# Kernel tuning notes

Hardware: AMD Instinct MI355X
Metric: run time of the kernel (lower is better)

## Reference

```python
import jax, jax.numpy as jnp
import numpy as np

N_GRAPHS = 128
N_NODES = 512
N = N_GRAPHS * N_NODES      # 65536 total nodes
E = 524288                  # edges (avg degree 8)
F_IN = 4                    # num_features
EMB = 4                     # embedding_dim
HEADS = 4
GDIM = 16                   # GATConv_dim
D = GDIM * HEADS            # 64 = d_model
NHEAD = 2                   # heads // 2
FF = 64                     # ff_hid_dim
OUT = 64                    # output_dim
N_GAT_REST = 3              # gat_layers - 1


def setup_inputs() -> dict:
    key = jax.random.key(0)
    ks = iter(jax.random.split(key, 64))
    def nrm(shape, fan_in):
        return jax.random.normal(next(ks), shape, jnp.float32) / np.float32(np.sqrt(fan_in))
    inp = {}
    inp['x'] = jax.random.normal(next(ks), (N, F_IN), jnp.float32)
    inp['edge_index'] = jax.random.randint(next(ks), (2, E), 0, N, dtype=jnp.int32)
    inp['batch'] = jnp.repeat(jnp.arange(N_GRAPHS, dtype=jnp.int32), N_NODES)
    # feature_fc
    inp['Wf'] = nrm((F_IN, EMB), F_IN); inp['bf'] = jnp.zeros((EMB,), jnp.float32)
    # input GATConv (EMB -> HEADS*GDIM)
    inp['gW0'] = nrm((EMB, HEADS * GDIM), EMB)
    inp['aS0'] = nrm((HEADS, GDIM), GDIM); inp['aD0'] = nrm((HEADS, GDIM), GDIM)
    inp['gb0'] = jnp.zeros((D,), jnp.float32)
    # remaining 3 GATConv layers (D -> HEADS*GDIM), stacked
    inp['gW'] = nrm((N_GAT_REST, D, HEADS * GDIM), D)
    inp['aS'] = nrm((N_GAT_REST, HEADS, GDIM), GDIM); inp['aD'] = nrm((N_GAT_REST, HEADS, GDIM), GDIM)
    inp['gb'] = jnp.zeros((N_GAT_REST, D), jnp.float32)
    # decoder layer: self-attn, cross-attn, layernorms, FFN
    for p in ['sWq','sWk','sWv','sWo','cWq','cWk','cWv','cWo']:
        inp[p] = nrm((D, D), D)
    for p in ['sbq','sbk','sbv','sbo','cbq','cbk','cbv','cbo']:
        inp[p] = jnp.zeros((D,), jnp.float32)
    for g, b in [('ln1g','ln1b'), ('ln2g','ln2b'), ('ln3g','ln3b')]:
        inp[g] = jnp.ones((D,), jnp.float32); inp[b] = jnp.zeros((D,), jnp.float32)
    inp['ffW1'] = nrm((D, FF), D); inp['ffb1'] = jnp.zeros((FF,), jnp.float32)
    inp['ffW2'] = nrm((FF, D), FF); inp['ffb2'] = jnp.zeros((D,), jnp.float32)
    inp['fcW'] = nrm((D, OUT), D); inp['fcb'] = jnp.zeros((OUT,), jnp.float32)
    return inp


def _gat(h_in, src, dst, W, a_s, a_d, b):
    # PyG GATConv, concat=True, negative_slope=0.2, self-loops already in (src,dst)
    h = (h_in @ W).reshape(N, HEADS, GDIM)
    es = jnp.einsum('nho,ho->nh', h, a_s)   # [N,H]
    ed = jnp.einsum('nho,ho->nh', h, a_d)
    e = jax.nn.leaky_relu(es[src] + ed[dst], 0.2)          # [E',H]
    m = jax.ops.segment_max(e, dst, num_segments=N)        # segment softmax over dst
    w = jnp.exp(e - m[dst])
    s = jax.ops.segment_sum(w, dst, num_segments=N)
    alpha = w / (s[dst] + 1e-16)
    out = jax.ops.segment_sum(h[src] * alpha[..., None], dst, num_segments=N)
    return out.reshape(N, D) + b


def _mha(q, kv, Wq, bq, Wk, bk, Wv, bv, Wo, bo):
    B, S, Dm = q.shape
    hd = Dm // NHEAD
    Q = (q @ Wq + bq).reshape(B, S, NHEAD, hd)
    K = (kv @ Wk + bk).reshape(B, S, NHEAD, hd)
    V = (kv @ Wv + bv).reshape(B, S, NHEAD, hd)
    a = jax.nn.softmax(jnp.einsum('bqhd,bkhd->bhqk', Q, K) / jnp.sqrt(jnp.float32(hd)), axis=-1)
    o = jnp.einsum('bhqk,bkhd->bqhd', a, V).reshape(B, S, Dm)
    return o @ Wo + bo


def _ln(x, g, b):
    m = x.mean(-1, keepdims=True)
    v = ((x - m) ** 2).mean(-1, keepdims=True)
    return (x - m) / jnp.sqrt(v + 1e-5) * g + b


def reference(x, edge_index, batch, Wf, bf, gW0, aS0, aD0, gb0, gW, aS, aD, gb,
              sWq, sWk, sWv, sWo, cWq, cWk, cWv, cWo,
              sbq, sbk, sbv, sbo, cbq, cbk, cbv, cbo,
              ln1g, ln1b, ln2g, ln2b, ln3g, ln3b,
              ffW1, ffb1, ffW2, ffb2, fcW, fcb):
    loops = jnp.arange(N, dtype=edge_index.dtype)
    src = jnp.concatenate([edge_index[0], loops])
    dst = jnp.concatenate([edge_index[1], loops])
    h = x @ Wf + bf
    h = jax.nn.leaky_relu(_gat(h, src, dst, gW0, aS0, aD0, gb0), 0.01)
    for i in range(N_GAT_REST):
        h = jax.nn.leaky_relu(_gat(h, src, dst, gW[i], aS[i], aD[i], gb[i]), 0.01)
    t = h.reshape(N_GRAPHS, N_NODES, D)
    # one transformer decoder layer, post-norm, memory = layer input
    mem = t
    t = _ln(t + _mha(t, t, sWq, sbq, sWk, sbk, sWv, sbv, sWo, sbo), ln1g, ln1b)
    t = _ln(t + _mha(t, mem, cWq, cbq, cWk, cbk, cWv, cbv, cWo, cbo), ln2g, ln2b)
    t = _ln(t + (jax.nn.relu(t @ ffW1 + ffb1) @ ffW2 + ffb2), ln3g, ln3b)
    h = t.reshape(N, D)
    pooled = jax.ops.segment_sum(h, batch, num_segments=N_GRAPHS) / jnp.float32(N_NODES)
    return pooled @ fcW + fcb
```

## Files before the change

### kernel.cpp

```cpp
#include <hip/hip_runtime.h>
#include <math.h>

#define NG 128
#define SEQ 512
#define NN 65536
#define EE 524288
#define DM 64

typedef __attribute__((ext_vector_type(8))) short short8;
typedef __attribute__((ext_vector_type(4))) float f32x4;

__device__ __forceinline__ float lrelu(float x, float s){ return x > 0.f ? x : s*x; }

__device__ __forceinline__ unsigned short f2bf(float x){
  union { float f; unsigned u; } v; v.f = x;
  unsigned r = v.u + 0x7FFF + ((v.u>>16)&1);
  return (unsigned short)(r>>16);
}
__device__ __forceinline__ float bf2f(unsigned short x){
  union { unsigned u; float f; } v; v.u = ((unsigned)x)<<16;
  return v.f;
}

__global__ void k_count(const int* __restrict__ dst, int* __restrict__ deg){
  int e = blockIdx.x*256 + threadIdx.x;
  atomicAdd(&deg[dst[e]], 1);
}

__global__ void k_scan1(const int* __restrict__ deg, int* __restrict__ excl, int* __restrict__ bsums){
  __shared__ int sm[256];
  int tid = threadIdx.x;
  int i = blockIdx.x*256 + tid;
  int v = deg[i];
  sm[tid] = v;
  __syncthreads();
  int val = v;
  for (int off=1; off<256; off<<=1){
    int add = (tid>=off)? sm[tid-off] : 0;
    __syncthreads();
    val += add;
    sm[tid] = val;
    __syncthreads();
  }
  excl[i] = val - v;
  if (tid==255) bsums[blockIdx.x] = val;
}

__global__ void k_scan2(int* __restrict__ bsums){
  __shared__ int sm[256];
  int tid=threadIdx.x;
  int v = bsums[tid];
  sm[tid]=v;
  __syncthreads();
  int val=v;
  for (int off=1; off<256; off<<=1){
    int add = (tid>=off)? sm[tid-off]:0;
    __syncthreads();
    val += add;
    sm[tid]=val;
    __syncthreads();
  }
  bsums[tid] = val - v;
}

__global__ void k_scan3(const int* __restrict__ excl, const int* __restrict__ bsums,
                        int* __restrict__ rowp, int* __restrict__ cursor){
  int i = blockIdx.x*256 + threadIdx.x;
  int v = excl[i] + bsums[blockIdx.x];
  rowp[i]=v; cursor[i]=v;
  if (i==0) rowp[NN]=EE;
}

__global__ void k_fill(const int* __restrict__ src, const int* __restrict__ dst,
                       int* __restrict__ cursor, int* __restrict__ col){
  int e = blockIdx.x*256 + threadIdx.x;
  int d = dst[e];
  int p = atomicAdd(&cursor[d], 1);
  col[p] = src[e];
}

__global__ void k_w0(const float* __restrict__ Wf, const float* __restrict__ bf,
                     const float* __restrict__ gW0, float* __restrict__ W0c, float* __restrict__ b0c){
  int j = threadIdx.x;
  float b = 0.f;
  for (int k=0;k<4;k++) b += bf[k]*gW0[k*64+j];
  b0c[j]=b;
  for (int i=0;i<4;i++){
    float s=0.f;
    for(int k=0;k<4;k++) s += Wf[i*4+k]*gW0[k*64+j];
    W0c[i*64+j]=s;
  }
}

template<int DIN, int BIAS>
__global__ void __launch_bounds__(256) k_transform(const float* __restrict__ hin, const float* __restrict__ W,
                            const float* __restrict__ bias,
                            const float* __restrict__ aSp, const float* __restrict__ aDp,
                            unsigned short* __restrict__ hout, float* __restrict__ es, float* __restrict__ ed){
  __shared__ float inL[DIN][68];
  __shared__ float Wl[DIN][64];
  __shared__ float asl[64], adl[64];
  int tid = threadIdx.x;
  int n0 = blockIdx.x*64;
  if (tid < 64){ asl[tid] = aSp[tid]; adl[tid] = aDp[tid]; }
  for (int idx=tid; idx<DIN*16; idx+=256){
    int k = idx>>4, jj = (idx&15)<<2;
    *(float4*)&Wl[k][jj] = *(const float4*)&W[k*64+jj];
  }
  for (int idx=tid; idx<64*(DIN/4); idx+=256){
    int node = idx/(DIN/4), kk = (idx%(DIN/4))*4;
    float4 v = *(const float4*)&hin[(size_t)(n0+node)*DIN + kk];
    inL[kk][node]=v.x; inL[kk+1][node]=v.y; inL[kk+2][node]=v.z; inL[kk+3][node]=v.w;
  }
  __syncthreads();
  int i = tid>>4, j = tid&15;
  float acc[4][4];
  #pragma unroll
  for (int r=0;r<4;r++){
    #pragma unroll
    for (int c=0;c<4;c++) acc[r][c] = 0.f;
  }
  #pragma unroll 4
  for (int k=0;k<DIN;k++){
    float4 av = *(float4*)&inL[k][4*i];
    float4 bv = *(float4*)&Wl[k][4*j];
    float a_[4]={av.x,av.y,av.z,av.w}, b_[4]={bv.x,bv.y,bv.z,bv.w};
    #pragma unroll
    for (int r=0;r<4;r++){
      #pragma unroll
      for (int c=0;c<4;c++) acc[r][c] += a_[r]*b_[c];
    }
  }
  float4 asv = *(float4*)&asl[4*j];
  float4 adv = *(float4*)&adl[4*j];
  float bb[4] = {0.f,0.f,0.f,0.f};
  if (BIAS){
    float4 bv = *(const float4*)&bias[4*j];
    bb[0]=bv.x; bb[1]=bv.y; bb[2]=bv.z; bb[3]=bv.w;
  }
  #pragma unroll
  for (int r=0;r<4;r++){
    float y0=acc[r][0]+bb[0], y1=acc[r][1]+bb[1], y2=acc[r][2]+bb[2], y3=acc[r][3]+bb[3];
    int node = n0 + 4*i + r;
    ushort4 hv;
    hv.x=f2bf(y0); hv.y=f2bf(y1); hv.z=f2bf(y2); hv.w=f2bf(y3);
    *(ushort4*)&hout[(size_t)node*64 + 4*j] = hv;
    float ps = y0*asv.x + y1*asv.y + y2*asv.z + y3*asv.w;
    float pd = y0*adv.x + y1*adv.y + y2*adv.z + y3*adv.w;
    ps += __shfl_xor(ps,1); ps += __shfl_xor(ps,2);
    pd += __shfl_xor(pd,1); pd += __shfl_xor(pd,2);
    if ((j&3)==0){
      es[(size_t)node*4 + (j>>2)] = ps;
      ed[(size_t)node*4 + (j>>2)] = pd;
    }
  }
}

__global__ void __launch_bounds__(256) k_aggregate(const unsigned short* __restrict__ h, const float* __restrict__ es,
                            const float* __restrict__ ed, const int* __restrict__ rowp,
                            const int* __restrict__ col, const float* __restrict__ gb,
                            float* __restrict__ hout){
  int tid = threadIdx.x;
  int n = blockIdx.x*4 + (tid>>6);
  int lane = tid&63;
  int hh = lane>>4;
  float edn = ed[(size_t)n*4 + hh];
  int beg = rowp[n], end = rowp[n+1];
  float m = lrelu(es[(size_t)n*4+hh] + edn, 0.2f);
  float ssum = 1.f;
  float acc = bf2f(h[(size_t)n*64 + lane]);
  int i = beg;
  for (; i+4 <= end; i += 4){
    int s0 = col[i], s1 = col[i+1], s2 = col[i+2], s3 = col[i+3];
    float hv0 = bf2f(h[(size_t)s0*64 + lane]);
    float hv1 = bf2f(h[(size_t)s1*64 + lane]);
    float hv2 = bf2f(h[(size_t)s2*64 + lane]);
    float hv3 = bf2f(h[(size_t)s3*64 + lane]);
    float e0 = lrelu(es[(size_t)s0*4+hh] + edn, 0.2f);
    float e1 = lrelu(es[(size_t)s1*4+hh] + edn, 0.2f);
    float e2 = lrelu(es[(size_t)s2*4+hh] + edn, 0.2f);
    float e3 = lrelu(es[(size_t)s3*4+hh] + edn, 0.2f);
    float mx = fmaxf(fmaxf(e0,e1), fmaxf(e2,e3));
    if (mx > m + 8.f){
      float corr = __expf(m - mx);
      ssum *= corr; acc *= corr; m = mx;
    }
    float w0 = __expf(e0 - m), w1 = __expf(e1 - m);
    float w2 = __expf(e2 - m), w3 = __expf(e3 - m);
    ssum += (w0 + w1) + (w2 + w3);
    acc += (w0*hv0 + w1*hv1) + (w2*hv2 + w3*hv3);
  }
  for (; i < end; i++){
    int s0 = col[i];
    float hv0 = bf2f(h[(size_t)s0*64 + lane]);
    float e0 = lrelu(es[(size_t)s0*4+hh] + edn, 0.2f);
    if (e0 > m + 8.f){
      float corr = __expf(m - e0);
      ssum *= corr; acc *= corr; m = e0;
    }
    float w0 = __expf(e0 - m);
    ssum += w0;
    acc += w0*hv0;
  }
  float o = acc/(ssum + 1e-16f) + gb[lane];
  hout[(size_t)n*64 + lane] = lrelu(o, 0.01f);
}

template<int ACT>
__global__ void __launch_bounds__(256) k_linear(const float* __restrict__ in, const float* __restrict__ W,
                         const float* __restrict__ b, float* __restrict__ out){
  __shared__ float inL[64][68];
  __shared__ float Wl[64][64];
  int tid = threadIdx.x;
  int n0 = blockIdx.x*64;
  for (int idx=tid; idx<1024; idx+=256){
    int k = idx>>4, jj = (idx&15)<<2;
    *(float4*)&Wl[k][jj] = *(const float4*)&W[k*64+jj];
  }
  for (int idx=tid; idx<1024; idx+=256){
    int node = idx>>4, kk = (idx&15)<<2;
    float4 v = *(const float4*)&in[(size_t)(n0+node)*64 + kk];
    inL[kk][node]=v.x; inL[kk+1][node]=v.y; inL[kk+2][node]=v.z; inL[kk+3][node]=v.w;
  }
  __syncthreads();
  int i = tid>>4, j = tid&15;
  float acc[4][4];
  #pragma unroll
  for (int r=0;r<4;r++){
    #pragma unroll
    for (int c=0;c<4;c++) acc[r][c] = 0.f;
  }
  #pragma unroll 4
  for (int k=0;k<64;k++){
    float4 av = *(float4*)&inL[k][4*i];
    float4 bv = *(float4*)&Wl[k][4*j];
    float a_[4]={av.x,av.y,av.z,av.w}, b_[4]={bv.x,bv.y,bv.z,bv.w};
    #pragma unroll
    for (int r=0;r<4;r++){
      #pragma unroll
      for (int c=0;c<4;c++) acc[r][c] += a_[r]*b_[c];
    }
  }
  float4 bv = *(const float4*)&b[4*j];
  float bb[4] = {bv.x, bv.y, bv.z, bv.w};
  #pragma unroll
  for (int r=0;r<4;r++){
    float y[4];
    #pragma unroll
    for (int c=0;c<4;c++){
      y[c] = acc[r][c] + bb[c];
      if (ACT==1) y[c] = fmaxf(y[c], 0.f);
    }
    *(float4*)&out[(size_t)(n0+4*i+r)*64 + 4*j] = make_float4(y[0],y[1],y[2],y[3]);
  }
}

__global__ void __launch_bounds__(256) k_qkv(const float* __restrict__ in,
                      const float* __restrict__ W0, const float* __restrict__ b0, float* __restrict__ o0,
                      const float* __restrict__ W1, const float* __restrict__ b1, float* __restrict__ o1,
                      const float* __restrict__ W2, const float* __restrict__ b2, float* __restrict__ o2){
  __shared__ float inL[64][68];
  __shared__ float Wl[64][64];
  int tid = threadIdx.x;
  int n0 = blockIdx.x*64;
  for (int idx=tid; idx<1024; idx+=256){
    int node = idx>>4, kk = (idx&15)<<2;
    float4 v = *(const float4*)&in[(size_t)(n0+node)*64 + kk];
    inL[kk][node]=v.x; inL[kk+1][node]=v.y; inL[kk+2][node]=v.z; inL[kk+3][node]=v.w;
  }
  int i = tid>>4, j = tid&15;
  const float* Ws[3] = {W0, W1, W2};
  const float* bs[3] = {b0, b1, b2};
  float* os[3] = {o0, o1, o2};
  for (int w=0; w<3; w++){
    __syncthreads();
    for (int idx=tid; idx<1024; idx+=256){
      int k = idx>>4, jj = (idx&15)<<2;
      *(float4*)&Wl[k][jj] = *(const float4*)&Ws[w][k*64+jj];
    }
    __syncthreads();
    float acc[4][4];
    #pragma unroll
    for (int r=0;r<4;r++){
      #pragma unroll
      for (int c=0;c<4;c++) acc[r][c] = 0.f;
    }
    #pragma unroll 4
    for (int k=0;k<64;k++){
      float4 av = *(float4*)&inL[k][4*i];
      float4 bv = *(float4*)&Wl[k][4*j];
      float a_[4]={av.x,av.y,av.z,av.w}, b_[4]={bv.x,bv.y,bv.z,bv.w};
      #pragma unroll
      for (int r=0;r<4;r++){
        #pragma unroll
        for (int c=0;c<4;c++) acc[r][c] += a_[r]*b_[c];
      }
    }
    float4 bv = *(const float4*)&bs[w][4*j];
    float bb[4] = {bv.x, bv.y, bv.z, bv.w};
    #pragma unroll
    for (int r=0;r<4;r++){
      *(float4*)&os[w][(size_t)(n0+4*i+r)*64 + 4*j] =
        make_float4(acc[r][0]+bb[0], acc[r][1]+bb[1], acc[r][2]+bb[2], acc[r][3]+bb[3]);
    }
  }
}

__global__ void __launch_bounds__(256) k_kv(const float* __restrict__ in,
                     const float* __restrict__ W0, const float* __restrict__ b0, float* __restrict__ o0,
                     const float* __restrict__ W1, const float* __restrict__ b1, float* __restrict__ o1){
  __shared__ float inL[64][68];
  __shared__ float Wl[64][64];
  int tid = threadIdx.x;
  int n0 = blockIdx.x*64;
  for (int idx=tid; idx<1024; idx+=256){
    int node = idx>>4, kk = (idx&15)<<2;
    float4 v = *(const float4*)&in[(size_t)(n0+node)*64 + kk];
    inL[kk][node]=v.x; inL[kk+1][node]=v.y; inL[kk+2][node]=v.z; inL[kk+3][node]=v.w;
  }
  int i = tid>>4, j = tid&15;
  const float* Ws[2] = {W0, W1};
  const float* bs[2] = {b0, b1};
  float* os[2] = {o0, o1};
  for (int w=0; w<2; w++){
    __syncthreads();
    for (int idx=tid; idx<1024; idx+=256){
      int k = idx>>4, jj = (idx&15)<<2;
      *(float4*)&Wl[k][jj] = *(const float4*)&Ws[w][k*64+jj];
    }
    __syncthreads();
    float acc[4][4];
    #pragma unroll
    for (int r=0;r<4;r++){
      #pragma unroll
      for (int c=0;c<4;c++) acc[r][c] = 0.f;
    }
    #pragma unroll 4
    for (int k=0;k<64;k++){
      float4 av = *(float4*)&inL[k][4*i];
      float4 bv = *(float4*)&Wl[k][4*j];
      float a_[4]={av.x,av.y,av.z,av.w}, b_[4]={bv.x,bv.y,bv.z,bv.w};
      #pragma unroll
      for (int r=0;r<4;r++){
        #pragma unroll
        for (int c=0;c<4;c++) acc[r][c] += a_[r]*b_[c];
      }
    }
    float4 bv = *(const float4*)&bs[w][4*j];
    float bb[4] = {bv.x, bv.y, bv.z, bv.w};
    #pragma unroll
    for (int r=0;r<4;r++){
      *(float4*)&os[w][(size_t)(n0+4*i+r)*64 + 4*j] =
        make_float4(acc[r][0]+bb[0], acc[r][1]+bb[1], acc[r][2]+bb[2], acc[r][3]+bb[3]);
    }
  }
}

__global__ void __launch_bounds__(256) k_linear_resln(const float* __restrict__ in, const float* __restrict__ W,
                               const float* __restrict__ b, const float* __restrict__ res,
                               const float* __restrict__ g, const float* __restrict__ bl,
                               float* __restrict__ out){
  __shared__ float inL[64][68];
  __shared__ float Wl[64][64];
  int tid = threadIdx.x;
  int n0 = blockIdx.x*64;
  for (int idx=tid; idx<1024; idx+=256){
    int k = idx>>4, jj = (idx&15)<<2;
    *(float4*)&Wl[k][jj] = *(const float4*)&W[k*64+jj];
  }
  for (int idx=tid; idx<1024; idx+=256){
    int node = idx>>4, kk = (idx&15)<<2;
    float4 v = *(const float4*)&in[(size_t)(n0+node)*64 + kk];
    inL[kk][node]=v.x; inL[kk+1][node]=v.y; inL[kk+2][node]=v.z; inL[kk+3][node]=v.w;
  }
  __syncthreads();
  int i = tid>>4, j = tid&15;
  float acc[4][4];
  #pragma unroll
  for (int r=0;r<4;r++){
    #pragma unroll
    for (int c=0;c<4;c++) acc[r][c] = 0.f;
  }
  #pragma unroll 4
  for (int k=0;k<64;k++){
    float4 av = *(float4*)&inL[k][4*i];
    float4 bv = *(float4*)&Wl[k][4*j];
    float a_[4]={av.x,av.y,av.z,av.w}, b_[4]={bv.x,bv.y,bv.z,bv.w};
    #pragma unroll
    for (int r=0;r<4;r++){
      #pragma unroll
      for (int c=0;c<4;c++) acc[r][c] += a_[r]*b_[c];
    }
  }
  float4 bv = *(const float4*)&b[4*j];
  float bb[4] = {bv.x, bv.y, bv.z, bv.w};
  float4 gv = *(const float4*)&g[4*j];
  float4 blv = *(const float4*)&bl[4*j];
  float gg[4] = {gv.x, gv.y, gv.z, gv.w};
  float bb2[4] = {blv.x, blv.y, blv.z, blv.w};
  #pragma unroll
  for (int r=0;r<4;r++){
    int node = n0 + 4*i + r;
    float4 rv = *(const float4*)&res[(size_t)node*64 + 4*j];
    float y[4] = {acc[r][0]+bb[0]+rv.x, acc[r][1]+bb[1]+rv.y,
                  acc[r][2]+bb[2]+rv.z, acc[r][3]+bb[3]+rv.w};
    float s = (y[0]+y[1]) + (y[2]+y[3]);
    s += __shfl_xor(s,1); s += __shfl_xor(s,2); s += __shfl_xor(s,4); s += __shfl_xor(s,8);
    float mean = s * (1.f/64.f);
    float d[4] = {y[0]-mean, y[1]-mean, y[2]-mean, y[3]-mean};
    float v = (d[0]*d[0]+d[1]*d[1]) + (d[2]*d[2]+d[3]*d[3]);
    v += __shfl_xor(v,1); v += __shfl_xor(v,2); v += __shfl_xor(v,4); v += __shfl_xor(v,8);
    float inv = rsqrtf(v*(1.f/64.f) + 1e-5f);
    *(float4*)&out[(size_t)node*64 + 4*j] =
      make_float4(d[0]*inv*gg[0]+bb2[0], d[1]*inv*gg[1]+bb2[1],
                  d[2]*inv*gg[2]+bb2[2], d[3]*inv*gg[3]+bb2[3]);
  }
}

__global__ void __launch_bounds__(512, 4) k_attn(const float* __restrict__ Q, const float* __restrict__ K,
                      const float* __restrict__ V, float* __restrict__ Out){
  __shared__ char smem[40960];
  char* Ksm = smem;
  char* Vsm = smem + 16384;
  char* Psm = smem + 32768;

  int bid = blockIdx.x;
  int qh = bid & 1;
  int h  = (bid>>1) & 1;
  int b  = bid>>2;
  int tid = threadIdx.x;
  int wave = tid>>6;
  int l = tid & 63;
  int lq = l & 15;
  int g  = l >> 4;
  const float scale = 0.17677669529663687f;
  const size_t hb = (size_t)b*SEQ*64 + (size_t)h*32;
  const f32x4 zero = {0.f,0.f,0.f,0.f};

  int qbase = qh*256 + wave*32;
  short8 qf[2];
  f32x4 O[2][2];
  float m_[2], l_[2];
  #pragma unroll
  for (int qt=0; qt<2; qt++){
    const float* qp = Q + hb + (size_t)(qbase + qt*16 + lq)*64 + g*8;
    float4 a = *(const float4*)qp;
    float4 c = *(const float4*)(qp+4);
    union { short8 v; unsigned short u[8]; } uu;
    uu.u[0]=f2bf(a.x*scale); uu.u[1]=f2bf(a.y*scale); uu.u[2]=f2bf(a.z*scale); uu.u[3]=f2bf(a.w*scale);
    uu.u[4]=f2bf(c.x*scale); uu.u[5]=f2bf(c.y*scale); uu.u[6]=f2bf(c.z*scale); uu.u[7]=f2bf(c.w*scale);
    qf[qt] = uu.v;
    O[qt][0] = zero; O[qt][1] = zero;
    m_[qt] = -1e30f; l_[qt] = 0.f;
  }

  char* Pw = Psm + wave*1024;

  for (int ph=0; ph<2; ph++){
    __syncthreads();
    #pragma unroll
    for (int it=0; it<4; it++){
      int i = tid + it*512;
      int row = i>>3, j = i&7;
      const float* kp = K + hb + (size_t)(ph*256 + row)*64 + j*4;
      float4 v4 = *(const float4*)kp;
      uint2 w;
      w.x = (unsigned)f2bf(v4.x) | ((unsigned)f2bf(v4.y)<<16);
      w.y = (unsigned)f2bf(v4.z) | ((unsigned)f2bf(v4.w)<<16);
      *(uint2*)(Ksm + row*64 + ((j*8) ^ (((row>>1)&3)<<4))) = w;
    }
    #pragma unroll
    for (int it=0; it<4; it++){
      int i = tid + it*512;
      int key = i>>3, j = i&7;
      const float* vp = V + hb + (size_t)(ph*256 + key)*64 + j*4;
      float4 v4 = *(const float4*)vp;
      float vv[4] = {v4.x, v4.y, v4.z, v4.w};
      #pragma unroll
      for (int c=0;c<4;c++){
        int d = j*4 + c;
        *(unsigned short*)(Vsm + d*512 + ((key*2) ^ ((d&7)<<4))) = f2bf(vv[c]);
      }
    }
    __syncthreads();
    for (int p=0; p<8; p++){
      int r0 = p*32 + lq, r1 = r0 + 16;
      short8 kf0 = *(short8*)(Ksm + r0*64 + ((g*16) ^ (((r0>>1)&3)<<4)));
      short8 kf1 = *(short8*)(Ksm + r1*64 + ((g*16) ^ (((r1>>1)&3)<<4)));
      int d0 = lq, d1 = lq + 16;
      short8 vt0 = *(short8*)(Vsm + d0*512 + ((p*64 + g*16) ^ ((d0&7)<<4)));
      short8 vt1 = *(short8*)(Vsm + d1*512 + ((p*64 + g*16) ^ ((d1&7)<<4)));
      int swzp = ((lq>>1)&3)<<4;
      #pragma unroll
      for (int qt=0; qt<2; qt++){
        f32x4 s0 = __builtin_amdgcn_mfma_f32_16x16x32_bf16(kf0, qf[qt], zero, 0,0,0);
        f32x4 s1 = __builtin_amdgcn_mfma_f32_16x16x32_bf16(kf1, qf[qt], zero, 0,0,0);
        float pmax = fmaxf(fmaxf(fmaxf(s0.x,s0.y),fmaxf(s0.z,s0.w)),
                           fmaxf(fmaxf(s1.x,s1.y),fmaxf(s1.z,s1.w)));
        pmax = fmaxf(pmax, __shfl_xor(pmax, 16));
        pmax = fmaxf(pmax, __shfl_xor(pmax, 32));
        float mn = fmaxf(m_[qt], pmax);
        float corr = __expf(m_[qt] - mn);
        m_[qt] = mn;
        float e0 = __expf(s0.x - mn), e1 = __expf(s0.y - mn);
        float e2 = __expf(s0.z - mn), e3 = __expf(s0.w - mn);
        float e4 = __expf(s1.x - mn), e5 = __expf(s1.y - mn);
        float e6 = __expf(s1.z - mn), e7 = __expf(s1.w - mn);
        l_[qt] = l_[qt]*corr + (((e0+e1)+(e2+e3)) + ((e4+e5)+(e6+e7)));
        O[qt][0] *= corr; O[qt][1] *= corr;
        uint2 w0, w1;
        w0.x = (unsigned)f2bf(e0) | ((unsigned)f2bf(e1)<<16);
        w0.y = (unsigned)f2bf(e2) | ((unsigned)f2bf(e3)<<16);
        w1.x = (unsigned)f2bf(e4) | ((unsigned)f2bf(e5)<<16);
        w1.y = (unsigned)f2bf(e6) | ((unsigned)f2bf(e7)<<16);
        *(uint2*)(Pw + lq*64 + ((g*8) ^ swzp)) = w0;
        *(uint2*)(Pw + lq*64 + ((32 + g*8) ^ swzp)) = w1;
        short8 pb = *(short8*)(Pw + lq*64 + ((g*16) ^ swzp));
        O[qt][0] = __builtin_amdgcn_mfma_f32_16x16x32_bf16(vt0, pb, O[qt][0], 0,0,0);
        O[qt][1] = __builtin_amdgcn_mfma_f32_16x16x32_bf16(vt1, pb, O[qt][1], 0,0,0);
      }
    }
  }
  #pragma unroll
  for (int qt=0; qt<2; qt++){
    float lt = l_[qt];
    lt += __shfl_xor(lt, 16);
    lt += __shfl_xor(lt, 32);
    float inv = 1.f/lt;
    float* op = Out + hb + (size_t)(qbase + qt*16 + lq)*64;
    float4 o0 = make_float4(O[qt][0].x*inv, O[qt][0].y*inv, O[qt][0].z*inv, O[qt][0].w*inv);
    float4 o1 = make_float4(O[qt][1].x*inv, O[qt][1].y*inv, O[qt][1].z*inv, O[qt][1].w*inv);
    *(float4*)(op + g*4) = o0;
    *(float4*)(op + 16 + g*4) = o1;
  }
}

__global__ void __launch_bounds__(256) k_pool_fc(const float* __restrict__ t, const float* __restrict__ fcW,
                          const float* __restrict__ fcb, float* __restrict__ out){
  __shared__ float pl[4][64];
  __shared__ float pf[64];
  int b = blockIdx.x;
  int tid = threadIdx.x;
  int j = tid&63, seg = tid>>6;
  const float* basep = t + (size_t)b*SEQ*64;
  float s = 0.f;
  for (int si=seg*128; si<(seg+1)*128; si++) s += basep[(size_t)si*64 + j];
  pl[seg][j] = s;
  __syncthreads();
  if (tid < 64){
    pf[tid] = (pl[0][tid]+pl[1][tid]+pl[2][tid]+pl[3][tid]) * (1.f/512.f);
  }
  __syncthreads();
  if (tid < 64){
    float o = fcb[tid];
    for (int k=0;k<64;k++) o += pf[k]*fcW[k*64+tid];
    out[(size_t)b*64 + tid] = o;
  }
}

extern "C" void kernel_launch(void* const* d_in, const int* in_sizes, int n_in,
                              void* d_out, int out_size, void* d_ws, size_t ws_size,
                              hipStream_t stream) {
  const float* x    = (const float*)d_in[0];
  const int*   ei   = (const int*)d_in[1];
  const float* Wf   = (const float*)d_in[3];
  const float* bf   = (const float*)d_in[4];
  const float* gW0  = (const float*)d_in[5];
  const float* aS0  = (const float*)d_in[6];
  const float* aD0  = (const float*)d_in[7];
  const float* gb0  = (const float*)d_in[8];
  const float* gW   = (const float*)d_in[9];
  const float* aS   = (const float*)d_in[10];
  const float* aD   = (const float*)d_in[11];
  const float* gb   = (const float*)d_in[12];
  const float* sWq  = (const float*)d_in[13];
  const float* sWk  = (const float*)d_in[14];
  const float* sWv  = (const float*)d_in[15];
  const float* sWo  = (const float*)d_in[16];
  const float* cWq  = (const float*)d_in[17];
  const float* cWk  = (const float*)d_in[18];
  const float* cWv  = (const float*)d_in[19];
  const float* cWo  = (const float*)d_in[20];
  const float* sbq  = (const float*)d_in[21];
  const float* sbk  = (const float*)d_in[22];
  const float* sbv  = (const float*)d_in[23];
  const float* sbo  = (const float*)d_in[24];
  const float* cbq  = (const float*)d_in[25];
  const float* cbk  = (const float*)d_in[26];
  const float* cbv  = (const float*)d_in[27];
  const float* cbo  = (const float*)d_in[28];
  const float* ln1g = (const float*)d_in[29];
  const float* ln1b = (const float*)d_in[30];
  const float* ln2g = (const float*)d_in[31];
  const float* ln2b = (const float*)d_in[32];
  const float* ln3g = (const float*)d_in[33];
  const float* ln3b = (const float*)d_in[34];
  const float* ffW1 = (const float*)d_in[35];
  const float* ffb1 = (const float*)d_in[36];
  const float* ffW2 = (const float*)d_in[37];
  const float* ffb2 = (const float*)d_in[38];
  const float* fcW  = (const float*)d_in[39];
  const float* fcb  = (const float*)d_in[40];

  char* ws = (char*)d_ws;
  size_t off = 0;
  auto alloc = [&](size_t bytes) -> void* {
    void* p = ws + off;
    off += (bytes + 255) & ~(size_t)255;
    return p;
  };
  int* deg    = (int*)alloc(NN*sizeof(int));
  int* excl   = (int*)alloc(NN*sizeof(int));
  int* rowp   = (int*)alloc((NN+1)*sizeof(int));
  int* cursor = (int*)alloc(NN*sizeof(int));
  int* col    = (int*)alloc(EE*sizeof(int));
  int* bsums  = (int*)alloc(256*sizeof(int));
  float* W0c  = (float*)alloc(4*64*sizeof(float));
  float* b0c  = (float*)alloc(64*sizeof(float));
  float* es   = (float*)alloc((size_t)NN*4*sizeof(float));
  float* ed   = (float*)alloc((size_t)NN*4*sizeof(float));
  unsigned short* Hb = (unsigned short*)alloc((size_t)NN*64*sizeof(unsigned short));
  float* B0   = (float*)alloc((size_t)NN*64*sizeof(float));
  float* B1   = (float*)alloc((size_t)NN*64*sizeof(float));
  float* B2   = (float*)alloc((size_t)NN*64*sizeof(float));
  float* B3   = (float*)alloc((size_t)NN*64*sizeof(float));
  float* B4   = (float*)alloc((size_t)NN*64*sizeof(float));
  float* B5   = (float*)alloc((size_t)NN*64*sizeof(float));

  const int* e_src = ei;
  const int* e_dst = ei + EE;

  hipMemsetAsync(deg, 0, NN*sizeof(int), stream);
  k_count<<<EE/256, 256, 0, stream>>>(e_dst, deg);
  k_scan1<<<NN/256, 256, 0, stream>>>(deg, excl, bsums);
  k_scan2<<<1, 256, 0, stream>>>(bsums);
  k_scan3<<<NN/256, 256, 0, stream>>>(excl, bsums, rowp, cursor);
  k_fill<<<EE/256, 256, 0, stream>>>(e_src, e_dst, cursor, col);

  k_w0<<<1, 64, 0, stream>>>(Wf, bf, gW0, W0c, b0c);

  k_transform<4,1><<<NN/64, 256, 0, stream>>>(x, W0c, b0c, aS0, aD0, Hb, es, ed);
  k_aggregate<<<NN/4, 256, 0, stream>>>(Hb, es, ed, rowp, col, gb0, B0);
  k_transform<64,0><<<NN/64, 256, 0, stream>>>(B0, gW+0*4096, nullptr, aS+0*64, aD+0*64, Hb, es, ed);
  k_aggregate<<<NN/4, 256, 0, stream>>>(Hb, es, ed, rowp, col, gb+0*64, B2);
  k_transform<64,0><<<NN/64, 256, 0, stream>>>(B2, gW+1*4096, nullptr, aS+1*64, aD+1*64, Hb, es, ed);
  k_aggregate<<<NN/4, 256, 0, stream>>>(Hb, es, ed, rowp, col, gb+1*64, B0);
  k_transform<64,0><<<NN/64, 256, 0, stream>>>(B0, gW+2*4096, nullptr, aS+2*64, aD+2*64, Hb, es, ed);
  k_aggregate<<<NN/4, 256, 0, stream>>>(Hb, es, ed, rowp, col, gb+2*64, B2);

  k_qkv<<<NN/64, 256, 0, stream>>>(B2, sWq, sbq, B0, sWk, sbk, B1, sWv, sbv, B3);
  k_attn<<<NG*2*2, 512, 0, stream>>>(B0, B1, B3, B4);
  k_linear_resln<<<NN/64, 256, 0, stream>>>(B4, sWo, sbo, B2, ln1g, ln1b, B5);

  k_linear<0><<<NN/64, 256, 0, stream>>>(B5, cWq, cbq, B0);
  k_kv<<<NN/64, 256, 0, stream>>>(B2, cWk, cbk, B1, cWv, cbv, B3);
  k_attn<<<NG*2*2, 512, 0, stream>>>(B0, B1, B3, B4);
  k_linear_resln<<<NN/64, 256, 0, stream>>>(B4, cWo, cbo, B5, ln2g, ln2b, B2);

  k_linear<1><<<NN/64, 256, 0, stream>>>(B2, ffW1, ffb1, B0);
  k_linear_resln<<<NN/64, 256, 0, stream>>>(B0, ffW2, ffb2, B2, ln3g, ln3b, B1);

  k_pool_fc<<<NG, 256, 0, stream>>>(B1, fcW, fcb, (float*)d_out);
}
```

Baseline: 453.8 us.

## Vectorize GAT aggregation across edges, keep intermediates bf16, merge cross-attn projections

The aggregation kernel now assigns four edge slots per wavefront, with 16 lanes each gathering four bf16 features as a ushort4. Partial online-softmax states are merged with shuffles, and the self-loop is folded in at the end. The three intermediate GAT layer outputs are written as bf16 and read by a new bf16-input transform kernel, which halves those memory round trips. The cross-attention Q projection and KV projection are merged into one generalized three-input projection kernel, removing a launch. The aim is fewer dependent gather latencies and less traffic, at the cost of extra bf16 rounding and idle lanes on low-degree nodes.

```diff
diff --git a/kernel.cpp b/kernel.cpp
--- a/kernel.cpp
+++ b/kernel.cpp
@@ -156,54 +156,147 @@
   }
 }
 
+__global__ void __launch_bounds__(256) k_transform_bf(const unsigned short* __restrict__ hin, const float* __restrict__ W,
+                            const float* __restrict__ aSp, const float* __restrict__ aDp,
+                            unsigned short* __restrict__ hout, float* __restrict__ es, float* __restrict__ ed){
+  __shared__ float inL[64][68];
+  __shared__ float Wl[64][64];
+  __shared__ float asl[64], adl[64];
+  int tid = threadIdx.x;
+  int n0 = blockIdx.x*64;
+  if (tid < 64){ asl[tid] = aSp[tid]; adl[tid] = aDp[tid]; }
+  for (int idx=tid; idx<1024; idx+=256){
+    int k = idx>>4, jj = (idx&15)<<2;
+    *(float4*)&Wl[k][jj] = *(const float4*)&W[k*64+jj];
+  }
+  for (int idx=tid; idx<1024; idx+=256){
+    int node = idx>>4, kk = (idx&15)<<2;
+    ushort4 v = *(const ushort4*)&hin[(size_t)(n0+node)*64 + kk];
+    inL[kk][node]=bf2f(v.x); inL[kk+1][node]=bf2f(v.y); inL[kk+2][node]=bf2f(v.z); inL[kk+3][node]=bf2f(v.w);
+  }
+  __syncthreads();
+  int i = tid>>4, j = tid&15;
+  float acc[4][4];
+  #pragma unroll
+  for (int r=0;r<4;r++){
+    #pragma unroll
+    for (int c=0;c<4;c++) acc[r][c] = 0.f;
+  }
+  #pragma unroll 4
+  for (int k=0;k<64;k++){
+    float4 av = *(float4*)&inL[k][4*i];
+    float4 bv = *(float4*)&Wl[k][4*j];
+    float a_[4]={av.x,av.y,av.z,av.w}, b_[4]={bv.x,bv.y,bv.z,bv.w};
+    #pragma unroll
+    for (int r=0;r<4;r++){
+      #pragma unroll
+      for (int c=0;c<4;c++) acc[r][c] += a_[r]*b_[c];
+    }
+  }
+  float4 asv = *(float4*)&asl[4*j];
+  float4 adv = *(float4*)&adl[4*j];
+  #pragma unroll
+  for (int r=0;r<4;r++){
+    float y0=acc[r][0], y1=acc[r][1], y2=acc[r][2], y3=acc[r][3];
+    int node = n0 + 4*i + r;
+    ushort4 hv;
+    hv.x=f2bf(y0); hv.y=f2bf(y1); hv.z=f2bf(y2); hv.w=f2bf(y3);
+    *(ushort4*)&hout[(size_t)node*64 + 4*j] = hv;
+    float ps = y0*asv.x + y1*asv.y + y2*asv.z + y3*asv.w;
+    float pd = y0*adv.x + y1*adv.y + y2*adv.z + y3*adv.w;
+    ps += __shfl_xor(ps,1); ps += __shfl_xor(ps,2);
+    pd += __shfl_xor(pd,1); pd += __shfl_xor(pd,2);
+    if ((j&3)==0){
+      es[(size_t)node*4 + (j>>2)] = ps;
+      ed[(size_t)node*4 + (j>>2)] = pd;
+    }
+  }
+}
+
+template<int BF16OUT>
 __global__ void __launch_bounds__(256) k_aggregate(const unsigned short* __restrict__ h, const float* __restrict__ es,
                             const float* __restrict__ ed, const int* __restrict__ rowp,
                             const int* __restrict__ col, const float* __restrict__ gb,
-                            float* __restrict__ hout){
+                            void* __restrict__ houtv){
   int tid = threadIdx.x;
   int n = blockIdx.x*4 + (tid>>6);
-  int lane = tid&63;
-  int hh = lane>>4;
-  float edn = ed[(size_t)n*4 + hh];
+  int l = tid&63;
+  int q = l>>4;
+  int sl = l&15;
+  int head = sl>>2;
+  float edn = ed[(size_t)n*4 + head];
+  float es_self = es[(size_t)n*4 + head];
   int beg = rowp[n], end = rowp[n+1];
-  float m = lrelu(es[(size_t)n*4+hh] + edn, 0.2f);
-  float ssum = 1.f;
-  float acc = bf2f(h[(size_t)n*64 + lane]);
-  int i = beg;
-  for (; i+4 <= end; i += 4){
-    int s0 = col[i], s1 = col[i+1], s2 = col[i+2], s3 = col[i+3];
-    float hv0 = bf2f(h[(size_t)s0*64 + lane]);
-    float hv1 = bf2f(h[(size_t)s1*64 + lane]);
-    float hv2 = bf2f(h[(size_t)s2*64 + lane]);
-    float hv3 = bf2f(h[(size_t)s3*64 + lane]);
-    float e0 = lrelu(es[(size_t)s0*4+hh] + edn, 0.2f);
-    float e1 = lrelu(es[(size_t)s1*4+hh] + edn, 0.2f);
-    float e2 = lrelu(es[(size_t)s2*4+hh] + edn, 0.2f);
-    float e3 = lrelu(es[(size_t)s3*4+hh] + edn, 0.2f);
-    float mx = fmaxf(fmaxf(e0,e1), fmaxf(e2,e3));
-    if (mx > m + 8.f){
-      float corr = __expf(m - mx);
-      ssum *= corr; acc *= corr; m = mx;
-    }
-    float w0 = __expf(e0 - m), w1 = __expf(e1 - m);
-    float w2 = __expf(e2 - m), w3 = __expf(e3 - m);
-    ssum += (w0 + w1) + (w2 + w3);
-    acc += (w0*hv0 + w1*hv1) + (w2*hv2 + w3*hv3);
-  }
-  for (; i < end; i++){
-    int s0 = col[i];
-    float hv0 = bf2f(h[(size_t)s0*64 + lane]);
-    float e0 = lrelu(es[(size_t)s0*4+hh] + edn, 0.2f);
-    if (e0 > m + 8.f){
-      float corr = __expf(m - e0);
-      ssum *= corr; acc *= corr; m = e0;
-    }
-    float w0 = __expf(e0 - m);
-    ssum += w0;
-    acc += w0*hv0;
-  }
-  float o = acc/(ssum + 1e-16f) + gb[lane];
-  hout[(size_t)n*64 + lane] = lrelu(o, 0.01f);
+  float m = -1e30f, s = 0.f;
+  float a0=0.f, a1=0.f, a2=0.f, a3=0.f;
+  for (int i=beg; i<end; i+=8){
+    int ei0 = i + q, ei1 = i + 4 + q;
+    bool ac0 = ei0 < end, ac1 = ei1 < end;
+    int i0 = ac0 ? ei0 : end-1;
+    int i1 = ac1 ? ei1 : end-1;
+    int s0 = col[i0], s1 = col[i1];
+    ushort4 hv0 = *(const ushort4*)&h[(size_t)s0*64 + 4*sl];
+    ushort4 hv1 = *(const ushort4*)&h[(size_t)s1*64 + 4*sl];
+    float e0 = lrelu(es[(size_t)s0*4+head] + edn, 0.2f);
+    float e1 = lrelu(es[(size_t)s1*4+head] + edn, 0.2f);
+    if (!ac0) e0 = -1e30f;
+    if (!ac1) e1 = -1e30f;
+    float mx = fmaxf(e0, e1);
+    if (__any(mx > m + 8.f)){
+      float nm = fmaxf(m, mx);
+      float c = __expf(m - nm);
+      s*=c; a0*=c; a1*=c; a2*=c; a3*=c; m = nm;
+    }
+    float w0 = ac0 ? __expf(e0 - m) : 0.f;
+    float w1 = ac1 ? __expf(e1 - m) : 0.f;
+    s += w0 + w1;
+    a0 += w0*bf2f(hv0.x) + w1*bf2f(hv1.x);
+    a1 += w0*bf2f(hv0.y) + w1*bf2f(hv1.y);
+    a2 += w0*bf2f(hv0.z) + w1*bf2f(hv1.z);
+    a3 += w0*bf2f(hv0.w) + w1*bf2f(hv1.w);
+  }
+  #pragma unroll
+  for (int off=16; off<=32; off<<=1){
+    float m2 = __shfl_xor(m, off);
+    float s2 = __shfl_xor(s, off);
+    float b0 = __shfl_xor(a0, off);
+    float b1 = __shfl_xor(a1, off);
+    float b2 = __shfl_xor(a2, off);
+    float b3 = __shfl_xor(a3, off);
+    float nm = fmaxf(m, m2);
+    float c1 = __expf(m - nm), c2 = __expf(m2 - nm);
+    s  = s*c1  + s2*c2;
+    a0 = a0*c1 + b0*c2;
+    a1 = a1*c1 + b1*c2;
+    a2 = a2*c1 + b2*c2;
+    a3 = a3*c1 + b3*c2;
+    m = nm;
+  }
+  {
+    float e_self = lrelu(es_self + edn, 0.2f);
+    float nm = fmaxf(m, e_self);
+    float c = __expf(m - nm), cs = __expf(e_self - nm);
+    ushort4 hs = *(const ushort4*)&h[(size_t)n*64 + 4*sl];
+    s  = s*c  + cs;
+    a0 = a0*c + cs*bf2f(hs.x);
+    a1 = a1*c + cs*bf2f(hs.y);
+    a2 = a2*c + cs*bf2f(hs.z);
+    a3 = a3*c + cs*bf2f(hs.w);
+  }
+  if (q == 0){
+    float inv = 1.f/(s + 1e-16f);
+    float4 gv = *(const float4*)&gb[4*sl];
+    float o0 = lrelu(a0*inv + gv.x, 0.01f);
+    float o1 = lrelu(a1*inv + gv.y, 0.01f);
+    float o2 = lrelu(a2*inv + gv.z, 0.01f);
+    float o3 = lrelu(a3*inv + gv.w, 0.01f);
+    if (BF16OUT){
+      ushort4 hv; hv.x=f2bf(o0); hv.y=f2bf(o1); hv.z=f2bf(o2); hv.w=f2bf(o3);
+      *(ushort4*)((unsigned short*)houtv + (size_t)n*64 + 4*sl) = hv;
+    } else {
+      *(float4*)((float*)houtv + (size_t)n*64 + 4*sl) = make_float4(o0,o1,o2,o3);
+    }
+  }
 }
 
 template<int ACT>
@@ -255,75 +348,29 @@
   }
 }
 
-__global__ void __launch_bounds__(256) k_qkv(const float* __restrict__ in,
-                      const float* __restrict__ W0, const float* __restrict__ b0, float* __restrict__ o0,
-                      const float* __restrict__ W1, const float* __restrict__ b1, float* __restrict__ o1,
-                      const float* __restrict__ W2, const float* __restrict__ b2, float* __restrict__ o2){
+__global__ void __launch_bounds__(256) k_qkv3(const float* __restrict__ in0, const float* __restrict__ W0, const float* __restrict__ b0, float* __restrict__ o0,
+                      const float* __restrict__ in1, const float* __restrict__ W1, const float* __restrict__ b1, float* __restrict__ o1,
+                      const float* __restrict__ in2, const float* __restrict__ W2, const float* __restrict__ b2, float* __restrict__ o2){
   __shared__ float inL[64][68];
   __shared__ float Wl[64][64];
   int tid = threadIdx.x;
   int n0 = blockIdx.x*64;
-  for (int idx=tid; idx<1024; idx+=256){
-    int node = idx>>4, kk = (idx&15)<<2;
-    float4 v = *(const float4*)&in[(size_t)(n0+node)*64 + kk];
-    inL[kk][node]=v.x; inL[kk+1][node]=v.y; inL[kk+2][node]=v.z; inL[kk+3][node]=v.w;
-  }
   int i = tid>>4, j = tid&15;
+  const float* ins[3] = {in0, in1, in2};
   const float* Ws[3] = {W0, W1, W2};
   const float* bs[3] = {b0, b1, b2};
   float* os[3] = {o0, o1, o2};
+  const float* cur = nullptr;
   for (int w=0; w<3; w++){
     __syncthreads();
-    for (int idx=tid; idx<1024; idx+=256){
-      int k = idx>>4, jj = (idx&15)<<2;
-      *(float4*)&Wl[k][jj] = *(const float4*)&Ws[w][k*64+jj];
-    }
-    __syncthreads();
-    float acc[4][4];
-    #pragma unroll
-    for (int r=0;r<4;r++){
-      #pragma unroll
-      for (int c=0;c<4;c++) acc[r][c] = 0.f;
-    }
-    #pragma unroll 4
-    for (int k=0;k<64;k++){
-      float4 av = *(float4*)&inL[k][4*i];
-      float4 bv = *(float4*)&Wl[k][4*j];
-      float a_[4]={av.x,av.y,av.z,av.w}, b_[4]={bv.x,bv.y,bv.z,bv.w};
-      #pragma unroll
-      for (int r=0;r<4;r++){
-        #pragma unroll
-        for (int c=0;c<4;c++) acc[r][c] += a_[r]*b_[c];
+    if (ins[w] != cur){
+      cur = ins[w];
+      for (int idx=tid; idx<1024; idx+=256){
+        int node = idx>>4, kk = (idx&15)<<2;
+        float4 v = *(const float4*)&cur[(size_t)(n0+node)*64 + kk];
+        inL[kk][node]=v.x; inL[kk+1][node]=v.y; inL[kk+2][node]=v.z; inL[kk+3][node]=v.w;
       }
     }
-    float4 bv = *(const float4*)&bs[w][4*j];
-    float bb[4] = {bv.x, bv.y, bv.z, bv.w};
-    #pragma unroll
-    for (int r=0;r<4;r++){
-      *(float4*)&os[w][(size_t)(n0+4*i+r)*64 + 4*j] =
-        make_float4(acc[r][0]+bb[0], acc[r][1]+bb[1], acc[r][2]+bb[2], acc[r][3]+bb[3]);
-    }
-  }
-}
-
-__global__ void __launch_bounds__(256) k_kv(const float* __restrict__ in,
-                     const float* __restrict__ W0, const float* __restrict__ b0, float* __restrict__ o0,
-                     const float* __restrict__ W1, const float* __restrict__ b1, float* __restrict__ o1){
-  __shared__ float inL[64][68];
-  __shared__ float Wl[64][64];
-  int tid = threadIdx.x;
-  int n0 = blockIdx.x*64;
-  for (int idx=tid; idx<1024; idx+=256){
-    int node = idx>>4, kk = (idx&15)<<2;
-    float4 v = *(const float4*)&in[(size_t)(n0+node)*64 + kk];
-    inL[kk][node]=v.x; inL[kk+1][node]=v.y; inL[kk+2][node]=v.z; inL[kk+3][node]=v.w;
-  }
-  int i = tid>>4, j = tid&15;
-  const float* Ws[2] = {W0, W1};
-  const float* bs[2] = {b0, b1};
-  float* os[2] = {o0, o1};
-  for (int w=0; w<2; w++){
-    __syncthreads();
     for (int idx=tid; idx<1024; idx+=256){
       int k = idx>>4, jj = (idx&15)<<2;
       *(float4*)&Wl[k][jj] = *(const float4*)&Ws[w][k*64+jj];
@@ -619,7 +666,8 @@
   float* b0c  = (float*)alloc(64*sizeof(float));
   float* es   = (float*)alloc((size_t)NN*4*sizeof(float));
   float* ed   = (float*)alloc((size_t)NN*4*sizeof(float));
-  unsigned short* Hb = (unsigned short*)alloc((size_t)NN*64*sizeof(unsigned short));
+  unsigned short* Hb   = (unsigned short*)alloc((size_t)NN*64*sizeof(unsigned short));
+  unsigned short* Hagg = (unsigned short*)alloc((size_t)NN*64*sizeof(unsigned short));
   float* B0   = (float*)alloc((size_t)NN*64*sizeof(float));
   float* B1   = (float*)alloc((size_t)NN*64*sizeof(float));
   float* B2   = (float*)alloc((size_t)NN*64*sizeof(float));
@@ -640,20 +688,19 @@
   k_w0<<<1, 64, 0, stream>>>(Wf, bf, gW0, W0c, b0c);
 
   k_transform<4,1><<<NN/64, 256, 0, stream>>>(x, W0c, b0c, aS0, aD0, Hb, es, ed);
-  k_aggregate<<<NN/4, 256, 0, stream>>>(Hb, es, ed, rowp, col, gb0, B0);
-  k_transform<64,0><<<NN/64, 256, 0, stream>>>(B0, gW+0*4096, nullptr, aS+0*64, aD+0*64, Hb, es, ed);
-  k_aggregate<<<NN/4, 256, 0, stream>>>(Hb, es, ed, rowp, col, gb+0*64, B2);
-  k_transform<64,0><<<NN/64, 256, 0, stream>>>(B2, gW+1*4096, nullptr, aS+1*64, aD+1*64, Hb, es, ed);
-  k_aggregate<<<NN/4, 256, 0, stream>>>(Hb, es, ed, rowp, col, gb+1*64, B0);
-  k_transform<64,0><<<NN/64, 256, 0, stream>>>(B0, gW+2*4096, nullptr, aS+2*64, aD+2*64, Hb, es, ed);
-  k_aggregate<<<NN/4, 256, 0, stream>>>(Hb, es, ed, rowp, col, gb+2*64, B2);
-
-  k_qkv<<<NN/64, 256, 0, stream>>>(B2, sWq, sbq, B0, sWk, sbk, B1, sWv, sbv, B3);
+  k_aggregate<1><<<NN/4, 256, 0, stream>>>(Hb, es, ed, rowp, col, gb0, Hagg);
+  k_transform_bf<<<NN/64, 256, 0, stream>>>(Hagg, gW+0*4096, aS+0*64, aD+0*64, Hb, es, ed);
+  k_aggregate<1><<<NN/4, 256, 0, stream>>>(Hb, es, ed, rowp, col, gb+0*64, Hagg);
+  k_transform_bf<<<NN/64, 256, 0, stream>>>(Hagg, gW+1*4096, aS+1*64, aD+1*64, Hb, es, ed);
+  k_aggregate<1><<<NN/4, 256, 0, stream>>>(Hb, es, ed, rowp, col, gb+1*64, Hagg);
+  k_transform_bf<<<NN/64, 256, 0, stream>>>(Hagg, gW+2*4096, aS+2*64, aD+2*64, Hb, es, ed);
+  k_aggregate<0><<<NN/4, 256, 0, stream>>>(Hb, es, ed, rowp, col, gb+2*64, B2);
+
+  k_qkv3<<<NN/64, 256, 0, stream>>>(B2, sWq, sbq, B0, B2, sWk, sbk, B1, B2, sWv, sbv, B3);
   k_attn<<<NG*2*2, 512, 0, stream>>>(B0, B1, B3, B4);
   k_linear_resln<<<NN/64, 256, 0, stream>>>(B4, sWo, sbo, B2, ln1g, ln1b, B5);
 
-  k_linear<0><<<NN/64, 256, 0, stream>>>(B5, cWq, cbq, B0);
-  k_kv<<<NN/64, 256, 0, stream>>>(B2, cWk, cbk, B1, cWv, cbv, B3);
+  k_qkv3<<<NN/64, 256, 0, stream>>>(B5, cWq, cbq, B0, B2, cWk, cbk, B1, B2, cWv, cbv, B3);
   k_attn<<<NG*2*2, 512, 0, stream>>>(B0, B1, B3, B4);
   k_linear_resln<<<NN/64, 256, 0, stream>>>(B4, cWo, cbo, B5, ln2g, ln2b, B2);
 
```

Measured after the change: 427.1 us. 1.06x faster.
